# Kernel optimization log

Hardware: AMD Instinct MI355X
Metric: run time of the kernel (lower is better)

The kernel has to match this reference:

```python
import jax, jax.numpy as jnp
import numpy as np

N = 50000       # nodes
E = 800000      # edges (avg degree 16)
D_IN = 128      # input_dim
HID = 128       # hidden_dim
G_FEAT = 32     # g_feat_dim
G = 64          # number of graphs in batch
EPS = 1e-5      # BatchNorm eps


def _lin_init(key, fan_in, fan_out):
    s = 1.0 / np.sqrt(fan_in)
    return jax.random.uniform(key, (fan_in, fan_out), jnp.float32, -s, s)


def setup_inputs() -> dict:
    key = jax.random.key(0)
    ks = jax.random.split(key, 24)
    inp = {
        'x': jax.random.normal(ks[0], (N, D_IN), jnp.float32),
        'edge_index': jax.random.randint(ks[1], (2, E), 0, N, jnp.int64),
        'batch': jnp.sort(jax.random.randint(ks[2], (N,), 0, G, jnp.int64)),
        'g_feats': jax.random.normal(ks[3], (G, G_FEAT), jnp.float32),
    }
    dims = [D_IN, HID, HID]
    k = 4
    for i, din in enumerate(dims):
        inp[f'Wl{i}'] = _lin_init(ks[k], din, HID); k += 1   # lin_l (neighbors, has bias)
        inp[f'bl{i}'] = jnp.zeros((HID,), jnp.float32)
        inp[f'Wr{i}'] = _lin_init(ks[k], din, HID); k += 1   # lin_r (self, no bias in PyG)
        inp[f'gamma{i}'] = jnp.ones((HID,), jnp.float32)
        inp[f'beta{i}'] = jnp.zeros((HID,), jnp.float32)
    inp['W1'] = _lin_init(ks[k], 2 * HID + G_FEAT, HID); k += 1
    inp['b1'] = jnp.zeros((HID,), jnp.float32)
    inp['W2'] = _lin_init(ks[k], HID, HID // 2); k += 1
    inp['b2'] = jnp.zeros((HID // 2,), jnp.float32)
    inp['W3'] = _lin_init(ks[k], HID // 2, 1); k += 1
    inp['b3'] = jnp.zeros((1,), jnp.float32)
    return inp


def _sage_conv(h, src, dst, Wl, bl, Wr):
    # mean-aggregate neighbor messages x_j into target i, then lin_l(agg)+lin_r(self)
    msgs = h[src]  # [E, d] irregular gather
    agg = jax.ops.segment_sum(msgs, dst, num_segments=N)
    cnt = jax.ops.segment_sum(jnp.ones((E,), h.dtype), dst, num_segments=N)
    agg = agg / jnp.clip(cnt, 1.0)[:, None]
    return agg @ Wl + bl + h @ Wr


def _batch_norm(h, gamma, beta):
    mu = jnp.mean(h, axis=0)
    var = jnp.var(h, axis=0)
    return gamma * (h - mu) * jax.lax.rsqrt(var + EPS) + beta


def _forward(x, edge_index, batch, g_feats, convs, head):
    src, dst = edge_index[0], edge_index[1]
    h = x
    for (Wl, bl, Wr, gamma, beta) in convs:
        h = jax.nn.relu(_batch_norm(_sage_conv(h, src, dst, Wl, bl, Wr), gamma, beta))
        # dropout p=0.01: identity in eval/reference mode
    cnt = jnp.clip(jax.ops.segment_sum(jnp.ones((N,), h.dtype), batch, num_segments=G), 1.0)
    hg_mean = jax.ops.segment_sum(h, batch, num_segments=G) / cnt[:, None]
    hg_max = jax.ops.segment_max(h, batch, num_segments=G)
    W1, b1, W2, b2, W3, b3 = head
    m = jnp.concatenate([hg_mean, hg_max, g_feats], axis=1)  # [G, 2*HID+G_FEAT]
    m = jax.nn.relu(m @ W1 + b1)
    m = jax.nn.relu(m @ W2 + b2)
    return (m @ W3 + b3).reshape(-1)  # [G]


def reference(x, edge_index, batch, g_feats,
              Wl0, bl0, Wr0, gamma0, beta0,
              Wl1, bl1, Wr1, gamma1, beta1,
              Wl2, bl2, Wr2, gamma2, beta2,
              W1, b1, W2, b2, W3, b3):
    convs = [(Wl0, bl0, Wr0, gamma0, beta0),
             (Wl1, bl1, Wr1, gamma1, beta1),
             (Wl2, bl2, Wr2, gamma2, beta2)]
    head = (W1, b1, W2, b2, W3, b3)
    return _forward(x, edge_index, batch, g_feats, convs, head)
```

## Files before the change

### kernel.cpp

```cpp
#include <hip/hip_runtime.h>
#include <stdint.h>

#define NN 50000
#define NE 800000
#define HID 128
#define NG 64
#define BN_EPS 1e-5f
#define SCAN_BLOCKS 196
#define GEMM_BLOCKS ((NN + 127) / 128)
#define SC_NB 8
#define SC_BSZ ((NN + SC_NB - 1) / SC_NB)
#define SC_CHUNK 4096
#define SC_CHUNKS ((NE + SC_CHUNK - 1) / SC_CHUNK)

typedef __bf16 bf16x8 __attribute__((ext_vector_type(8)));
typedef float floatx4 __attribute__((ext_vector_type(4)));

__device__ __forceinline__ float b2f(unsigned short u) {
    union { unsigned int i; float f; } x; x.i = ((unsigned int)u) << 16; return x.f;
}
__device__ __forceinline__ float blo(unsigned int d) { return __uint_as_float(d << 16); }
__device__ __forceinline__ float bhi(unsigned int d) { return __uint_as_float(d & 0xffff0000u); }
__device__ __forceinline__ unsigned short f2b(float f) {
    union { float f; unsigned int i; } x; x.f = f; unsigned int i = x.i;
    if ((i & 0x7f800000u) == 0x7f800000u) return (unsigned short)(i >> 16);
    return (unsigned short)((i + 0x7fffu + ((i >> 16) & 1u)) >> 16);
}
__device__ __forceinline__ unsigned int pack2(float f0, float f1) {
    return (((unsigned int)f2b(f1)) << 16) | f2b(f0);
}
__device__ __forceinline__ float2 bn_pair(const float* __restrict__ bnstat,
                                          const float* __restrict__ gamma,
                                          const float* __restrict__ beta, int c) {
    float mu = bnstat[c] * (1.f / NN);
    float var = bnstat[128 + c] * (1.f / NN) - mu * mu;
    float s = gamma[c] * rsqrtf(var + BN_EPS);
    return make_float2(s, beta[c] - mu * s);
}

__global__ void k_setup(const float* __restrict__ x, unsigned short* xb, int* deg,
                        int* gstart, int* gend, float* bnstats,
                        float* pool_sum, int* pool_max,
                        const float* __restrict__ Wl0, const float* __restrict__ Wr0,
                        const float* __restrict__ Wl1, const float* __restrict__ Wr1,
                        const float* __restrict__ Wl2, const float* __restrict__ Wr2,
                        unsigned short* Bp) {
    int i = blockIdx.x * 256 + threadIdx.x;
    if (i < NN * 64) {
        float2 v = ((const float2*)x)[i];
        ((unsigned int*)xb)[i] = pack2(v.x, v.y);
    }
    if (i < NN) deg[i] = 0;
    if (i < NG) { gstart[i] = NN; gend[i] = -1; }
    if (i < 3 * 256) bnstats[i] = 0.f;
    if (i < NG * HID) { pool_sum[i] = 0.f; pool_max[i] = 0; }
    if (i < 3 * 32768) {
        int layer = i >> 15;
        int r = i & 32767;
        int nt = r >> 12, kk = (r >> 9) & 7, l = (r >> 3) & 63, j = r & 7;
        int k = kk * 32 + (l >> 4) * 8 + j;
        int n = nt * 16 + (l & 15);
        const float* Wl = layer == 0 ? Wl0 : (layer == 1 ? Wl1 : Wl2);
        const float* Wr = layer == 0 ? Wr0 : (layer == 1 ? Wr1 : Wr2);
        Bp[i] = f2b((k < 128) ? Wl[k * 128 + n] : Wr[(k - 128) * 128 + n]);
    }
}

__global__ void k_hist(const int* __restrict__ dst, int* deg) {
    int bucket = blockIdx.x & (SC_NB - 1);
    int chunk = blockIdx.x / SC_NB;
    int lo = bucket * SC_BSZ, hi = lo + SC_BSZ;
    int base = chunk * SC_CHUNK;
#pragma unroll
    for (int i = 0; i < SC_CHUNK / 256; ++i) {
        int e = base + i * 256 + threadIdx.x;
        if (e < NE) {
            int d = dst[e];
            if (d >= lo && d < hi) atomicAdd(&deg[d], 1);
        }
    }
}

__global__ void k_scan1(const int* __restrict__ deg, int* blocksum,
                        const int* __restrict__ batch, int* gstart, int* gend) {
    __shared__ int lds[256];
    int t = threadIdx.x, i = blockIdx.x * 256 + t;
    lds[t] = (i < NN) ? deg[i] : 0;
    if (i < NN) {
        int g = batch[i];
        if (i == 0 || batch[i - 1] != g) atomicMin(&gstart[g], i);
        if (i == NN - 1 || batch[i + 1] != g) atomicMax(&gend[g], i);
    }
    __syncthreads();
    for (int off = 128; off > 0; off >>= 1) {
        if (t < off) lds[t] += lds[t + off];
        __syncthreads();
    }
    if (t == 0) blocksum[blockIdx.x] = lds[0];
}

__global__ void k_scan2(const int* __restrict__ blocksum, int* blockoff, int* row_start) {
    __shared__ int lds[256];
    int t = threadIdx.x;
    int v = (t < SCAN_BLOCKS) ? blocksum[t] : 0;
    lds[t] = v;
    __syncthreads();
    for (int off = 1; off < 256; off <<= 1) {
        int u = (t >= off) ? lds[t - off] : 0;
        __syncthreads();
        lds[t] += u;
        __syncthreads();
    }
    if (t < SCAN_BLOCKS) blockoff[t] = lds[t] - v;
    if (t == 255) row_start[NN] = lds[255];
}

__global__ void k_scan3(const int* __restrict__ deg, const int* __restrict__ blockoff,
                        int* row_start, int* cursor) {
    __shared__ int lds[256];
    int t = threadIdx.x, i = blockIdx.x * 256 + t;
    int v = (i < NN) ? deg[i] : 0;
    lds[t] = v;
    __syncthreads();
    for (int off = 1; off < 256; off <<= 1) {
        int u = (t >= off) ? lds[t - off] : 0;
        __syncthreads();
        lds[t] += u;
        __syncthreads();
    }
    if (i < NN) {
        int ex = blockoff[blockIdx.x] + lds[t] - v;
        row_start[i] = ex;
        cursor[i] = ex;
    }
}

__global__ void k_scatter(const int* __restrict__ src, const int* __restrict__ dst,
                          int* cursor, int* col) {
    int bucket = blockIdx.x & (SC_NB - 1);
    int chunk = blockIdx.x / SC_NB;
    int lo = bucket * SC_BSZ, hi = lo + SC_BSZ;
    int base = chunk * SC_CHUNK;
#pragma unroll
    for (int i = 0; i < SC_CHUNK / 256; ++i) {
        int e = base + i * 256 + threadIdx.x;
        if (e < NE) {
            int d = dst[e];
            if (d >= lo && d < hi) {
                int p = atomicAdd(&cursor[d], 1);
                col[p] = src[e];
            }
        }
    }
}

__global__ void k_agg(const unsigned short* __restrict__ h, const int* __restrict__ row_start,
                      const int* __restrict__ col, const float* __restrict__ bnstat,
                      const float* __restrict__ gamma, const float* __restrict__ beta,
                      unsigned short* __restrict__ agg) {
    int wid = threadIdx.x >> 6, lane = threadIdx.x & 63;
    int slot = lane >> 4, sub = lane & 15;
    int node = (blockIdx.x * 4 + wid) * 4 + slot;
    int s = row_start[node], e = row_start[node + 1];
    bool ap = bnstat != nullptr;
    float scv[8], shv[8];
    if (ap) {
#pragma unroll
        for (int i = 0; i < 8; ++i) {
            float2 p = bn_pair(bnstat, gamma, beta, sub * 8 + i);
            scv[i] = p.x; shv[i] = p.y;
        }
    }
    auto tf = [&](float f, int i) -> float {
        return ap ? fmaxf(f * scv[i] + shv[i], 0.f) : f;
    };
    const uint4* h4 = (const uint4*)h;
    float a0 = 0.f, a1 = 0.f, a2 = 0.f, a3 = 0.f, a4 = 0.f, a5 = 0.f, a6 = 0.f, a7 = 0.f;
    int j = s;
    for (; j + 4 <= e; j += 4) {
        int u0 = col[j], u1 = col[j + 1], u2 = col[j + 2], u3 = col[j + 3];
        uint4 v0 = h4[(size_t)u0 * 16 + sub];
        uint4 v1 = h4[(size_t)u1 * 16 + sub];
        uint4 v2 = h4[(size_t)u2 * 16 + sub];
        uint4 v3 = h4[(size_t)u3 * 16 + sub];
        a0 += (tf(blo(v0.x), 0) + tf(blo(v1.x), 0)) + (tf(blo(v2.x), 0) + tf(blo(v3.x), 0));
        a1 += (tf(bhi(v0.x), 1) + tf(bhi(v1.x), 1)) + (tf(bhi(v2.x), 1) + tf(bhi(v3.x), 1));
        a2 += (tf(blo(v0.y), 2) + tf(blo(v1.y), 2)) + (tf(blo(v2.y), 2) + tf(blo(v3.y), 2));
        a3 += (tf(bhi(v0.y), 3) + tf(bhi(v1.y), 3)) + (tf(bhi(v2.y), 3) + tf(bhi(v3.y), 3));
        a4 += (tf(blo(v0.z), 4) + tf(blo(v1.z), 4)) + (tf(blo(v2.z), 4) + tf(blo(v3.z), 4));
        a5 += (tf(bhi(v0.z), 5) + tf(bhi(v1.z), 5)) + (tf(bhi(v2.z), 5) + tf(bhi(v3.z), 5));
        a6 += (tf(blo(v0.w), 6) + tf(blo(v1.w), 6)) + (tf(blo(v2.w), 6) + tf(blo(v3.w), 6));
        a7 += (tf(bhi(v0.w), 7) + tf(bhi(v1.w), 7)) + (tf(bhi(v2.w), 7) + tf(bhi(v3.w), 7));
    }
    for (; j < e; ++j) {
        int u = col[j];
        uint4 v = h4[(size_t)u * 16 + sub];
        a0 += tf(blo(v.x), 0);  a1 += tf(bhi(v.x), 1);
        a2 += tf(blo(v.y), 2);  a3 += tf(bhi(v.y), 3);
        a4 += tf(blo(v.z), 4);  a5 += tf(bhi(v.z), 5);
        a6 += tf(blo(v.w), 6);  a7 += tf(bhi(v.w), 7);
    }
    float inv = (e > s) ? 1.f / (float)(e - s) : 0.f;
    uint4 o;
    o.x = pack2(a0 * inv, a1 * inv);
    o.y = pack2(a2 * inv, a3 * inv);
    o.z = pack2(a4 * inv, a5 * inv);
    o.w = pack2(a6 * inv, a7 * inv);
    ((uint4*)agg)[(size_t)node * 16 + sub] = o;
}

__device__ __forceinline__ bf16x8 norm8(bf16x8 v, const float* sc, const float* sh, int cbase) {
    union { bf16x8 v; unsigned short u[8]; } in; in.v = v;
    union { unsigned int u[4]; bf16x8 v; } out;
#pragma unroll
    for (int i = 0; i < 4; ++i) {
        float f0 = fmaxf(b2f(in.u[2 * i]) * sc[cbase + 2 * i] + sh[cbase + 2 * i], 0.f);
        float f1 = fmaxf(b2f(in.u[2 * i + 1]) * sc[cbase + 2 * i + 1] + sh[cbase + 2 * i + 1], 0.f);
        out.u[i] = pack2(f0, f1);
    }
    return out.v;
}

__global__ void __launch_bounds__(256) k_gemm(unsigned short* buf,
                                              const unsigned short* h,
                                              const unsigned short* __restrict__ Bp,
                                              const float* __restrict__ pbnstat,
                                              const float* __restrict__ pgamma,
                                              const float* __restrict__ pbeta,
                                              float* bnstat) {
    __shared__ unsigned short Bs[32768];
    __shared__ float s_sc[128], s_sh[128];
    int t = threadIdx.x;
    {
        const uint4* s4 = (const uint4*)Bp;
        uint4* d4 = (uint4*)Bs;
        for (int i = t; i < 4096; i += 256) d4[i] = s4[i];
    }
    bool ap = pbnstat != nullptr;
    if (ap && t < 128) {
        float2 p = bn_pair(pbnstat, pgamma, pbeta, t);
        s_sc[t] = p.x; s_sh[t] = p.y;
    }
    __syncthreads();
    int wid = t >> 6, lane = t & 63;
    int m = lane & 15, q = lane >> 4;
    int mbase = blockIdx.x * 128 + wid * 32;
    bool active = mbase < NN;
    float s8[8] = {0, 0, 0, 0, 0, 0, 0, 0};
    float ss8[8] = {0, 0, 0, 0, 0, 0, 0, 0};
    if (active) {
        int row0 = mbase + m;
        int row1 = min(mbase + 16 + m, NN - 1);
        const bf16x8* Abuf = (const bf16x8*)buf;
        const bf16x8* Ah = (const bf16x8*)h;
        size_t b0 = (size_t)row0 * 16, b1 = (size_t)row1 * 16;
        bf16x8 af0[8], af1[8];
#pragma unroll
        for (int kk = 0; kk < 4; ++kk) {
            af0[kk] = Abuf[b0 + kk * 4 + q];
            af1[kk] = Abuf[b1 + kk * 4 + q];
            bf16x8 h0 = Ah[b0 + kk * 4 + q];
            bf16x8 h1 = Ah[b1 + kk * 4 + q];
            if (ap) {
                int cb = kk * 32 + q * 8;
                h0 = norm8(h0, s_sc, s_sh, cb);
                h1 = norm8(h1, s_sc, s_sh, cb);
            }
            af0[4 + kk] = h0;
            af1[4 + kk] = h1;
        }
        const bf16x8* B = (const bf16x8*)Bs;
        floatx4 acc[2][8];
#pragma unroll
        for (int mt = 0; mt < 2; ++mt)
#pragma unroll
            for (int nt = 0; nt < 8; ++nt) acc[mt][nt] = (floatx4){0.f, 0.f, 0.f, 0.f};
#pragma unroll
        for (int kk = 0; kk < 8; ++kk) {
#pragma unroll
            for (int nt = 0; nt < 8; ++nt) {
                bf16x8 b = B[(nt * 8 + kk) * 64 + lane];
                acc[0][nt] = __builtin_amdgcn_mfma_f32_16x16x32_bf16(af0[kk], b, acc[0][nt], 0, 0, 0);
                acc[1][nt] = __builtin_amdgcn_mfma_f32_16x16x32_bf16(af1[kk], b, acc[1][nt], 0, 0, 0);
            }
        }
#pragma unroll
        for (int mt = 0; mt < 2; ++mt)
#pragma unroll
            for (int nt = 0; nt < 8; ++nt) {
                int c = nt * 16 + m;
#pragma unroll
                for (int reg = 0; reg < 4; ++reg) {
                    int r = mbase + mt * 16 + q * 4 + reg;
                    if (r < NN) {
                        float v = acc[mt][nt][reg];
                        buf[(size_t)r * 128 + c] = f2b(v);
                        s8[nt] += v;
                        ss8[nt] += v * v;
                    }
                }
            }
#pragma unroll
        for (int nt = 0; nt < 8; ++nt) {
            s8[nt] += __shfl_xor(s8[nt], 16, 64);  s8[nt] += __shfl_xor(s8[nt], 32, 64);
            ss8[nt] += __shfl_xor(ss8[nt], 16, 64); ss8[nt] += __shfl_xor(ss8[nt], 32, 64);
        }
    }
    __syncthreads();
    float* stf = (float*)Bs;
    if (t < 256) stf[t] = 0.f;
    __syncthreads();
    if (active && lane < 16) {
#pragma unroll
        for (int nt = 0; nt < 8; ++nt) {
            int c = nt * 16 + m;
            atomicAdd(&stf[c], s8[nt]);
            atomicAdd(&stf[128 + c], ss8[nt]);
        }
    }
    __syncthreads();
    if (t < 256) atomicAdd(&bnstat[t], stf[t]);
}

__global__ void k_pool(const unsigned short* __restrict__ h, const int* __restrict__ gstart,
                       const int* __restrict__ gend, const float* __restrict__ bnstat,
                       const float* __restrict__ gamma, const float* __restrict__ beta,
                       float* pool_sum, int* pool_max) {
    int g = blockIdx.x >> 3, chunk = blockIdx.x & 7;
    int s = gstart[g], e = gend[g];
    if (s > e) return;
    int cnt = e - s + 1;
    int per = (cnt + 7) >> 3;
    int r0 = s + chunk * per;
    int r1 = min(r0 + per, e + 1);
    int c = threadIdx.x & 127, half = threadIdx.x >> 7;
    float2 pr = bn_pair(bnstat, gamma, beta, c);
    float sm = 0.f, mx = 0.f;
    for (int r = r0 + half; r < r1; r += 2) {
        float v = fmaxf(b2f(h[(size_t)r * 128 + c]) * pr.x + pr.y, 0.f);
        sm += v;
        mx = fmaxf(mx, v);
    }
    atomicAdd(&pool_sum[g * 128 + c], sm);
    atomicMax(&pool_max[g * 128 + c], __float_as_int(mx));
}

__global__ void __launch_bounds__(128) k_head(
    const float* __restrict__ pool_sum, const int* __restrict__ pool_max,
    const int* __restrict__ gstart, const int* __restrict__ gend,
    const float* __restrict__ gfeats,
    const float* __restrict__ W1, const float* __restrict__ bs1,
    const float* __restrict__ W2, const float* __restrict__ bs2,
    const float* __restrict__ W3, const float* __restrict__ bs3,
    float* out) {
    __shared__ float m[288];
    __shared__ float o1[128];
    __shared__ float o2[64];
    int g = blockIdx.x, t = threadIdx.x;
    int s = gstart[g], e = gend[g];
    int cint = e - s + 1;
    float cnt = (float)(cint < 1 ? 1 : cint);
    if (t < 128) {
        m[t] = pool_sum[g * 128 + t] / cnt;
        m[128 + t] = __int_as_float(pool_max[g * 128 + t]);
    }
    if (t < 32) m[256 + t] = gfeats[g * 32 + t];
    __syncthreads();
    float acc = bs1[t];
    for (int k = 0; k < 288; ++k) acc += m[k] * W1[k * 128 + t];
    o1[t] = fmaxf(acc, 0.f);
    __syncthreads();
    if (t < 64) {
        float a2 = bs2[t];
        for (int k = 0; k < 128; ++k) a2 += o1[k] * W2[k * 64 + t];
        o2[t] = fmaxf(a2, 0.f);
    }
    __syncthreads();
    if (t < 64) {
        float p = o2[t] * W3[t];
#pragma unroll
        for (int off = 32; off; off >>= 1) p += __shfl_down(p, off, 64);
        if (t == 0) out[g] = p + bs3[0];
    }
}

extern "C" void kernel_launch(void* const* d_in, const int* in_sizes, int n_in,
                              void* d_out, int out_size, void* d_ws, size_t ws_size,
                              hipStream_t stream) {
    const float* x = (const float*)d_in[0];
    const int* ei = (const int*)d_in[1];
    const int* batch = (const int*)d_in[2];
    const float* gfeats = (const float*)d_in[3];
    const float *Wl[3], *Wr[3], *gma[3], *bta[3];
    for (int i = 0; i < 3; ++i) {
        Wl[i] = (const float*)d_in[4 + 5 * i];
        Wr[i] = (const float*)d_in[6 + 5 * i];
        gma[i] = (const float*)d_in[7 + 5 * i];
        bta[i] = (const float*)d_in[8 + 5 * i];
    }
    const float* W1 = (const float*)d_in[19];
    const float* bs1 = (const float*)d_in[20];
    const float* W2 = (const float*)d_in[21];
    const float* bs2 = (const float*)d_in[22];
    const float* W3 = (const float*)d_in[23];
    const float* bs3 = (const float*)d_in[24];

    char* p = (char*)d_ws;
    auto alloc = [&](size_t bytes) -> char* {
        char* r = p;
        p += (bytes + 255) & ~(size_t)255;
        return r;
    };
    int* deg = (int*)alloc(NN * 4);
    int* row_start = (int*)alloc((NN + 1) * 4);
    int* cursor = (int*)alloc(NN * 4);
    int* col = (int*)alloc(NE * 4);
    int* gstart = (int*)alloc(NG * 4);
    int* gend = (int*)alloc(NG * 4);
    float* bnstats = (float*)alloc(3 * 256 * 4);
    float* pool_sum = (float*)alloc(NG * HID * 4);
    int* pool_max = (int*)alloc(NG * HID * 4);
    int* blocksum = (int*)alloc(SCAN_BLOCKS * 4);
    int* blockoff = (int*)alloc(SCAN_BLOCKS * 4);
    unsigned short* Bp = (unsigned short*)alloc(3 * 32768 * 2);
    unsigned short* xb = (unsigned short*)alloc((size_t)NN * 128 * 2);
    unsigned short* b0 = (unsigned short*)alloc((size_t)NN * 128 * 2);
    unsigned short* b1 = (unsigned short*)alloc((size_t)NN * 128 * 2);

    const int* srcv = ei;
    const int* dstv = ei + NE;

    k_setup<<<(NN * 64 + 255) / 256, 256, 0, stream>>>(
        x, xb, deg, gstart, gend, bnstats, pool_sum, pool_max,
        Wl[0], Wr[0], Wl[1], Wr[1], Wl[2], Wr[2], Bp);
    k_hist<<<SC_CHUNKS * SC_NB, 256, 0, stream>>>(dstv, deg);
    k_scan1<<<SCAN_BLOCKS, 256, 0, stream>>>(deg, blocksum, batch, gstart, gend);
    k_scan2<<<1, 256, 0, stream>>>(blocksum, blockoff, row_start);
    k_scan3<<<SCAN_BLOCKS, 256, 0, stream>>>(deg, blockoff, row_start, cursor);
    k_scatter<<<SC_CHUNKS * SC_NB, 256, 0, stream>>>(srcv, dstv, cursor, col);

    const unsigned short* hin = xb;
    unsigned short* work[3] = {b0, b1, b0};
    for (int l = 0; l < 3; ++l) {
        unsigned short* w = work[l];
        const float* pb = (l == 0) ? nullptr : bnstats + (l - 1) * 256;
        const float* pg = (l == 0) ? nullptr : gma[l - 1];
        const float* pt = (l == 0) ? nullptr : bta[l - 1];
        k_agg<<<(NN + 15) / 16, 256, 0, stream>>>(hin, row_start, col, pb, pg, pt, w);
        k_gemm<<<GEMM_BLOCKS, 256, 0, stream>>>(w, hin, Bp + l * 32768, pb, pg, pt,
                                                bnstats + l * 256);
        hin = w;
    }
    k_pool<<<NG * 8, 256, 0, stream>>>(hin, gstart, gend, bnstats + 2 * 256, gma[2], bta[2],
                                       pool_sum, pool_max);
    k_head<<<NG, 128, 0, stream>>>(pool_sum, pool_max, gstart, gend, gfeats,
                                   W1, bs1, W2, bs2, W3, bs3, (float*)d_out);
}
```

Baseline: 399.5 us.

## Fuse neighbor aggregation and SAGE GEMM into one per-layer kernel

Merges the gather/mean aggregation kernel and the MFMA GEMM kernel into a single k_layer kernel. Each wave aggregates 16 nodes into shared memory and immediately uses them as the GEMM A operand, so the aggregated features no longer make a round trip through global memory and one launch per layer disappears. B weights are now read directly from global memory instead of being staged in LDS, and each wave handles 16 rows instead of 32. That means more blocks and more repeated B loads, and the GEMM no longer overlaps with other blocks' gathers as before.

New measurement: 476.4 us. 1.19x slower.

```diff
diff --git a/kernel.cpp b/kernel.cpp
--- a/kernel.cpp
+++ b/kernel.cpp
@@ -7,7 +7,7 @@
 #define NG 64
 #define BN_EPS 1e-5f
 #define SCAN_BLOCKS 196
-#define GEMM_BLOCKS ((NN + 127) / 128)
+#define LAYER_BLOCKS ((NN + 63) / 64)
 #define SC_NB 8
 #define SC_BSZ ((NN + SC_NB - 1) / SC_NB)
 #define SC_CHUNK 4096
@@ -154,61 +154,6 @@
     }
 }
 
-__global__ void k_agg(const unsigned short* __restrict__ h, const int* __restrict__ row_start,
-                      const int* __restrict__ col, const float* __restrict__ bnstat,
-                      const float* __restrict__ gamma, const float* __restrict__ beta,
-                      unsigned short* __restrict__ agg) {
-    int wid = threadIdx.x >> 6, lane = threadIdx.x & 63;
-    int slot = lane >> 4, sub = lane & 15;
-    int node = (blockIdx.x * 4 + wid) * 4 + slot;
-    int s = row_start[node], e = row_start[node + 1];
-    bool ap = bnstat != nullptr;
-    float scv[8], shv[8];
-    if (ap) {
-#pragma unroll
-        for (int i = 0; i < 8; ++i) {
-            float2 p = bn_pair(bnstat, gamma, beta, sub * 8 + i);
-            scv[i] = p.x; shv[i] = p.y;
-        }
-    }
-    auto tf = [&](float f, int i) -> float {
-        return ap ? fmaxf(f * scv[i] + shv[i], 0.f) : f;
-    };
-    const uint4* h4 = (const uint4*)h;
-    float a0 = 0.f, a1 = 0.f, a2 = 0.f, a3 = 0.f, a4 = 0.f, a5 = 0.f, a6 = 0.f, a7 = 0.f;
-    int j = s;
-    for (; j + 4 <= e; j += 4) {
-        int u0 = col[j], u1 = col[j + 1], u2 = col[j + 2], u3 = col[j + 3];
-        uint4 v0 = h4[(size_t)u0 * 16 + sub];
-        uint4 v1 = h4[(size_t)u1 * 16 + sub];
-        uint4 v2 = h4[(size_t)u2 * 16 + sub];
-        uint4 v3 = h4[(size_t)u3 * 16 + sub];
-        a0 += (tf(blo(v0.x), 0) + tf(blo(v1.x), 0)) + (tf(blo(v2.x), 0) + tf(blo(v3.x), 0));
-        a1 += (tf(bhi(v0.x), 1) + tf(bhi(v1.x), 1)) + (tf(bhi(v2.x), 1) + tf(bhi(v3.x), 1));
-        a2 += (tf(blo(v0.y), 2) + tf(blo(v1.y), 2)) + (tf(blo(v2.y), 2) + tf(blo(v3.y), 2));
-        a3 += (tf(bhi(v0.y), 3) + tf(bhi(v1.y), 3)) + (tf(bhi(v2.y), 3) + tf(bhi(v3.y), 3));
-        a4 += (tf(blo(v0.z), 4) + tf(blo(v1.z), 4)) + (tf(blo(v2.z), 4) + tf(blo(v3.z), 4));
-        a5 += (tf(bhi(v0.z), 5) + tf(bhi(v1.z), 5)) + (tf(bhi(v2.z), 5) + tf(bhi(v3.z), 5));
-        a6 += (tf(blo(v0.w), 6) + tf(blo(v1.w), 6)) + (tf(blo(v2.w), 6) + tf(blo(v3.w), 6));
-        a7 += (tf(bhi(v0.w), 7) + tf(bhi(v1.w), 7)) + (tf(bhi(v2.w), 7) + tf(bhi(v3.w), 7));
-    }
-    for (; j < e; ++j) {
-        int u = col[j];
-        uint4 v = h4[(size_t)u * 16 + sub];
-        a0 += tf(blo(v.x), 0);  a1 += tf(bhi(v.x), 1);
-        a2 += tf(blo(v.y), 2);  a3 += tf(bhi(v.y), 3);
-        a4 += tf(blo(v.z), 4);  a5 += tf(bhi(v.z), 5);
-        a6 += tf(blo(v.w), 6);  a7 += tf(bhi(v.w), 7);
-    }
-    float inv = (e > s) ? 1.f / (float)(e - s) : 0.f;
-    uint4 o;
-    o.x = pack2(a0 * inv, a1 * inv);
-    o.y = pack2(a2 * inv, a3 * inv);
-    o.z = pack2(a4 * inv, a5 * inv);
-    o.w = pack2(a6 * inv, a7 * inv);
-    ((uint4*)agg)[(size_t)node * 16 + sub] = o;
-}
-
 __device__ __forceinline__ bf16x8 norm8(bf16x8 v, const float* sc, const float* sh, int cbase) {
     union { bf16x8 v; unsigned short u[8]; } in; in.v = v;
     union { unsigned int u[4]; bf16x8 v; } out;
@@ -221,96 +166,128 @@
     return out.v;
 }
 
-__global__ void __launch_bounds__(256) k_gemm(unsigned short* buf,
-                                              const unsigned short* h,
-                                              const unsigned short* __restrict__ Bp,
-                                              const float* __restrict__ pbnstat,
-                                              const float* __restrict__ pgamma,
-                                              const float* __restrict__ pbeta,
-                                              float* bnstat) {
-    __shared__ unsigned short Bs[32768];
+__global__ void __launch_bounds__(256) k_layer(
+    const unsigned short* __restrict__ hin, const int* __restrict__ row_start,
+    const int* __restrict__ col, const unsigned short* __restrict__ Bp,
+    const float* __restrict__ pbnstat, const float* __restrict__ pgamma,
+    const float* __restrict__ pbeta,
+    unsigned short* __restrict__ out, float* __restrict__ bnstat) {
+    __shared__ uint4 Alds[4][16][17];
     __shared__ float s_sc[128], s_sh[128];
+    __shared__ float stf[256];
     int t = threadIdx.x;
-    {
-        const uint4* s4 = (const uint4*)Bp;
-        uint4* d4 = (uint4*)Bs;
-        for (int i = t; i < 4096; i += 256) d4[i] = s4[i];
-    }
     bool ap = pbnstat != nullptr;
     if (ap && t < 128) {
         float2 p = bn_pair(pbnstat, pgamma, pbeta, t);
         s_sc[t] = p.x; s_sh[t] = p.y;
     }
+    if (t < 256) stf[t] = 0.f;
     __syncthreads();
     int wid = t >> 6, lane = t & 63;
+    int wbase = blockIdx.x * 64 + wid * 16;
+
+    {
+        int slot = lane >> 4, sub = lane & 15;
+        float scv[8], shv[8];
+        if (ap) {
+#pragma unroll
+            for (int i = 0; i < 8; ++i) { scv[i] = s_sc[sub * 8 + i]; shv[i] = s_sh[sub * 8 + i]; }
+        }
+        auto tf = [&](float f, int i) -> float {
+            return ap ? fmaxf(f * scv[i] + shv[i], 0.f) : f;
+        };
+        const uint4* h4 = (const uint4*)hin;
+#pragma unroll 1
+        for (int r = 0; r < 4; ++r) {
+            int node = wbase + r * 4 + slot;
+            int s = 0, e = 0;
+            if (node < NN) { s = row_start[node]; e = row_start[node + 1]; }
+            float a0 = 0.f, a1 = 0.f, a2 = 0.f, a3 = 0.f, a4 = 0.f, a5 = 0.f, a6 = 0.f, a7 = 0.f;
+            int j = s;
+            for (; j + 4 <= e; j += 4) {
+                int u0 = col[j], u1 = col[j + 1], u2 = col[j + 2], u3 = col[j + 3];
+                uint4 v0 = h4[(size_t)u0 * 16 + sub];
+                uint4 v1 = h4[(size_t)u1 * 16 + sub];
+                uint4 v2 = h4[(size_t)u2 * 16 + sub];
+                uint4 v3 = h4[(size_t)u3 * 16 + sub];
+                a0 += (tf(blo(v0.x), 0) + tf(blo(v1.x), 0)) + (tf(blo(v2.x), 0) + tf(blo(v3.x), 0));
+                a1 += (tf(bhi(v0.x), 1) + tf(bhi(v1.x), 1)) + (tf(bhi(v2.x), 1) + tf(bhi(v3.x), 1));
+                a2 += (tf(blo(v0.y), 2) + tf(blo(v1.y), 2)) + (tf(blo(v2.y), 2) + tf(blo(v3.y), 2));
+                a3 += (tf(bhi(v0.y), 3) + tf(bhi(v1.y), 3)) + (tf(bhi(v2.y), 3) + tf(bhi(v3.y), 3));
+                a4 += (tf(blo(v0.z), 4) + tf(blo(v1.z), 4)) + (tf(blo(v2.z), 4) + tf(blo(v3.z), 4));
+                a5 += (tf(bhi(v0.z), 5) + tf(bhi(v1.z), 5)) + (tf(bhi(v2.z), 5) + tf(bhi(v3.z), 5));
+                a6 += (tf(blo(v0.w), 6) + tf(blo(v1.w), 6)) + (tf(blo(v2.w), 6) + tf(blo(v3.w), 6));
+                a7 += (tf(bhi(v0.w), 7) + tf(bhi(v1.w), 7)) + (tf(bhi(v2.w), 7) + tf(bhi(v3.w), 7));
+            }
+            for (; j < e; ++j) {
+                int u = col[j];
+                uint4 v = h4[(size_t)u * 16 + sub];
+                a0 += tf(blo(v.x), 0);  a1 += tf(bhi(v.x), 1);
+                a2 += tf(blo(v.y), 2);  a3 += tf(bhi(v.y), 3);
+                a4 += tf(blo(v.z), 4);  a5 += tf(bhi(v.z), 5);
+                a6 += tf(blo(v.w), 6);  a7 += tf(bhi(v.w), 7);
+            }
+            float inv = (e > s) ? 1.f / (float)(e - s) : 0.f;
+            uint4 o;
+            o.x = pack2(a0 * inv, a1 * inv);
+            o.y = pack2(a2 * inv, a3 * inv);
+            o.z = pack2(a4 * inv, a5 * inv);
+            o.w = pack2(a6 * inv, a7 * inv);
+            Alds[wid][r * 4 + slot][sub] = o;
+        }
+    }
+
     int m = lane & 15, q = lane >> 4;
-    int mbase = blockIdx.x * 128 + wid * 32;
-    bool active = mbase < NN;
+    int row = wbase + m;
+    int rowc = min(row, NN - 1);
+    bf16x8 af[8];
+#pragma unroll
+    for (int kk = 0; kk < 4; ++kk) {
+        uint4 a = Alds[wid][m][kk * 4 + q];
+        af[kk] = *(const bf16x8*)&a;
+    }
+    {
+        const bf16x8* hh = (const bf16x8*)hin + (size_t)rowc * 16;
+#pragma unroll
+        for (int kk = 0; kk < 4; ++kk) {
+            bf16x8 hv = hh[kk * 4 + q];
+            af[4 + kk] = ap ? norm8(hv, s_sc, s_sh, kk * 32 + q * 8) : hv;
+        }
+    }
+    const bf16x8* B = (const bf16x8*)Bp;
+    floatx4 acc[8];
+#pragma unroll
+    for (int nt = 0; nt < 8; ++nt) acc[nt] = (floatx4){0.f, 0.f, 0.f, 0.f};
+#pragma unroll
+    for (int kk = 0; kk < 8; ++kk) {
+#pragma unroll
+        for (int nt = 0; nt < 8; ++nt) {
+            bf16x8 b = B[(nt * 8 + kk) * 64 + lane];
+            acc[nt] = __builtin_amdgcn_mfma_f32_16x16x32_bf16(af[kk], b, acc[nt], 0, 0, 0);
+        }
+    }
     float s8[8] = {0, 0, 0, 0, 0, 0, 0, 0};
     float ss8[8] = {0, 0, 0, 0, 0, 0, 0, 0};
-    if (active) {
-        int row0 = mbase + m;
-        int row1 = min(mbase + 16 + m, NN - 1);
-        const bf16x8* Abuf = (const bf16x8*)buf;
-        const bf16x8* Ah = (const bf16x8*)h;
-        size_t b0 = (size_t)row0 * 16, b1 = (size_t)row1 * 16;
-        bf16x8 af0[8], af1[8];
-#pragma unroll
-        for (int kk = 0; kk < 4; ++kk) {
-            af0[kk] = Abuf[b0 + kk * 4 + q];
-            af1[kk] = Abuf[b1 + kk * 4 + q];
-            bf16x8 h0 = Ah[b0 + kk * 4 + q];
-            bf16x8 h1 = Ah[b1 + kk * 4 + q];
-            if (ap) {
-                int cb = kk * 32 + q * 8;
-                h0 = norm8(h0, s_sc, s_sh, cb);
-                h1 = norm8(h1, s_sc, s_sh, cb);
+#pragma unroll
+    for (int nt = 0; nt < 8; ++nt) {
+        int c = nt * 16 + m;
+#pragma unroll
+        for (int reg = 0; reg < 4; ++reg) {
+            int r = wbase + q * 4 + reg;
+            if (r < NN) {
+                float v = acc[nt][reg];
+                out[(size_t)r * 128 + c] = f2b(v);
+                s8[nt] += v;
+                ss8[nt] += v * v;
             }
-            af0[4 + kk] = h0;
-            af1[4 + kk] = h1;
-        }
-        const bf16x8* B = (const bf16x8*)Bs;
-        floatx4 acc[2][8];
-#pragma unroll
-        for (int mt = 0; mt < 2; ++mt)
-#pragma unroll
-            for (int nt = 0; nt < 8; ++nt) acc[mt][nt] = (floatx4){0.f, 0.f, 0.f, 0.f};
-#pragma unroll
-        for (int kk = 0; kk < 8; ++kk) {
-#pragma unroll
-            for (int nt = 0; nt < 8; ++nt) {
-                bf16x8 b = B[(nt * 8 + kk) * 64 + lane];
-                acc[0][nt] = __builtin_amdgcn_mfma_f32_16x16x32_bf16(af0[kk], b, acc[0][nt], 0, 0, 0);
-                acc[1][nt] = __builtin_amdgcn_mfma_f32_16x16x32_bf16(af1[kk], b, acc[1][nt], 0, 0, 0);
-            }
-        }
-#pragma unroll
-        for (int mt = 0; mt < 2; ++mt)
-#pragma unroll
-            for (int nt = 0; nt < 8; ++nt) {
-                int c = nt * 16 + m;
-#pragma unroll
-                for (int reg = 0; reg < 4; ++reg) {
-                    int r = mbase + mt * 16 + q * 4 + reg;
-                    if (r < NN) {
-                        float v = acc[mt][nt][reg];
-                        buf[(size_t)r * 128 + c] = f2b(v);
-                        s8[nt] += v;
-                        ss8[nt] += v * v;
-                    }
-                }
-            }
-#pragma unroll
-        for (int nt = 0; nt < 8; ++nt) {
-            s8[nt] += __shfl_xor(s8[nt], 16, 64);  s8[nt] += __shfl_xor(s8[nt], 32, 64);
-            ss8[nt] += __shfl_xor(ss8[nt], 16, 64); ss8[nt] += __shfl_xor(ss8[nt], 32, 64);
-        }
-    }
-    __syncthreads();
-    float* stf = (float*)Bs;
-    if (t < 256) stf[t] = 0.f;
-    __syncthreads();
-    if (active && lane < 16) {
+        }
+    }
+#pragma unroll
+    for (int nt = 0; nt < 8; ++nt) {
+        s8[nt] += __shfl_xor(s8[nt], 16, 64);  s8[nt] += __shfl_xor(s8[nt], 32, 64);
+        ss8[nt] += __shfl_xor(ss8[nt], 16, 64); ss8[nt] += __shfl_xor(ss8[nt], 32, 64);
+    }
+    if (lane < 16) {
 #pragma unroll
         for (int nt = 0; nt < 8; ++nt) {
             int c = nt * 16 + m;
@@ -446,9 +423,8 @@
         const float* pb = (l == 0) ? nullptr : bnstats + (l - 1) * 256;
         const float* pg = (l == 0) ? nullptr : gma[l - 1];
         const float* pt = (l == 0) ? nullptr : bta[l - 1];
-        k_agg<<<(NN + 15) / 16, 256, 0, stream>>>(hin, row_start, col, pb, pg, pt, w);
-        k_gemm<<<GEMM_BLOCKS, 256, 0, stream>>>(w, hin, Bp + l * 32768, pb, pg, pt,
-                                                bnstats + l * 256);
+        k_layer<<<LAYER_BLOCKS, 256, 0, stream>>>(hin, row_start, col, Bp + l * 32768,
+                                                  pb, pg, pt, w, bnstats + l * 256);
         hin = w;
     }
     k_pool<<<NG * 8, 256, 0, stream>>>(hin, gstart, gend, bnstats + 2 * 256, gma[2], bta[2],
```
